# Performance work log

Hardware: AMD Instinct MI355X
Metric: run time of the kernel (lower is better)

The kernel has to match this reference:

```python
import jax, jax.numpy as jnp
import numpy as np
from jax import lax

NUM_MELS = 80
NQ = 256          # num_quants
WIN = 1024
HOP = 256
K_UP = 800        # upsample kernel
PAD_UP = K_UP + 4 * HOP - WIN   # = 800
RC = 120          # residual_channels
SC = 240          # skip_channels
KC = 2            # causal kernel
NB = 16           # num blocks
DILS = [1, 2, 4, 8, 16, 32, 64, 128] * 2
DN = ('NCH', 'OIH', 'NCH')


def conv1x1(x, w, b):
    # x: [B,C,T], w: [O,C], b: [O]
    return jnp.einsum('bct,oc->bot', x, w) + b[None, :, None]


def causal_conv(x, w, b, d):
    # x: [B,RC,T], w: [2RC,RC,KC], left-pad by d*(KC-1) -> causal, same length
    y = lax.conv_general_dilated(x, w, (1,), [(d * (KC - 1), 0)],
                                 rhs_dilation=(d,), dimension_numbers=DN)
    return y + b[None, :, None]


def setup_inputs() -> dict:
    key = jax.random.key(0)
    ks = jax.random.split(key, 20)
    s = 0.05
    n = jax.random.normal
    return {
        'waveforms': n(ks[0], (1, 40960), jnp.float32),
        'melspecs': n(ks[1], (1, NUM_MELS, 160), jnp.float32),
        # ConvTranspose-equivalent upsample weight, stored as direct conv weight [O,I,K]
        'up_w': s * n(ks[2], (NUM_MELS, NUM_MELS, K_UP), jnp.float32),
        'up_b': jnp.zeros((NUM_MELS,), jnp.float32),
        'in_w': s * n(ks[3], (RC, 1), jnp.float32),
        'in_b': jnp.zeros((RC,), jnp.float32),
        'blk_causal_w': s * n(ks[4], (NB, 2 * RC, RC, KC), jnp.float32),
        'blk_causal_b': jnp.zeros((NB, 2 * RC), jnp.float32),
        'blk_cond_w': s * n(ks[5], (NB, 2 * RC, NUM_MELS), jnp.float32),
        'blk_cond_b': jnp.zeros((NB, 2 * RC), jnp.float32),
        'blk_skip_w': s * n(ks[6], (NB, SC, RC), jnp.float32),
        'blk_skip_b': jnp.zeros((NB, SC), jnp.float32),
        'blk_res_w': s * n(ks[7], (NB, RC, RC), jnp.float32),
        'blk_res_b': jnp.zeros((NB, RC), jnp.float32),
        'h1_w': s * n(ks[8], (NQ, SC), jnp.float32),
        'h1_b': jnp.zeros((NQ,), jnp.float32),
        'h2_w': s * n(ks[9], (NQ, NQ), jnp.float32),
        'h2_b': jnp.zeros((NQ,), jnp.float32),
    }


def _forward(waveforms, melspecs, up_w, up_b, in_w, in_b,
             blk_causal_w, blk_causal_b, blk_cond_w, blk_cond_b,
             blk_skip_w, blk_skip_b, blk_res_w, blk_res_b,
             h1_w, h1_b, h2_w, h2_b):
    # ConvTranspose1d(stride=HOP, padding=PAD_UP) as lhs-dilated conv:
    # out_len = (F-1)*HOP + K_UP - 2*PAD_UP
    cond = lax.conv_general_dilated(
        melspecs, up_w, (1,), [(K_UP - 1 - PAD_UP, K_UP - 1 - PAD_UP)],
        lhs_dilation=(HOP,), dimension_numbers=DN) + up_b[None, :, None]
    L = min(waveforms.shape[-1], cond.shape[-1])
    wav = waveforms[..., :L]
    cond = cond[..., :L]

    res = conv1x1(wav[:, None, :], in_w, in_b)          # [B,RC,L]
    skip_sum = jnp.zeros((res.shape[0], SC, L), res.dtype)
    for i, d in enumerate(DILS):
        z = causal_conv(res, blk_causal_w[i], blk_causal_b[i], d) \
            + conv1x1(cond, blk_cond_w[i], blk_cond_b[i])  # [B,2RC,L]
        h = jnp.tanh(z[:, :RC]) * jax.nn.sigmoid(z[:, RC:])
        skip_sum = skip_sum + conv1x1(h, blk_skip_w[i], blk_skip_b[i])
        res = res + conv1x1(h, blk_res_w[i], blk_res_b[i])

    x = jax.nn.relu(skip_sum)
    x = jax.nn.relu(conv1x1(x, h1_w, h1_b))
    logits = conv1x1(x, h2_w, h2_b)                      # [B,NQ,L]
    return logits


def reference(waveforms, melspecs, up_w, up_b, in_w, in_b,
              blk_causal_w, blk_causal_b, blk_cond_w, blk_cond_b,
              blk_skip_w, blk_skip_b, blk_res_w, blk_res_b,
              h1_w, h1_b, h2_w, h2_b):
    return _forward(waveforms, melspecs, up_w, up_b, in_w, in_b,
                    blk_causal_w, blk_causal_b, blk_cond_w, blk_cond_b,
                    blk_skip_w, blk_skip_b, blk_res_w, blk_res_b,
                    h1_w, h1_b, h2_w, h2_b)
```

## Files before the change

kernel.cpp:

```cpp
#include <hip/hip_runtime.h>

#define L_LEN 39904
#define NT 624
#define RCH 120
#define SCH 240
#define CMEL 80
#define NQO 256
#define NBLK 16
#define KUP 800

typedef unsigned short u16;
typedef __attribute__((ext_vector_type(8))) short short8;
typedef __attribute__((ext_vector_type(4))) float f32x4;

#define MFMA(a, b, c) __builtin_amdgcn_mfma_f32_16x16x32_bf16((a), (b), (c), 0, 0, 0)

__device__ __forceinline__ u16 f2bf(float f) {
    unsigned u = __float_as_uint(f);
    u += 0x7FFFu + ((u >> 16) & 1u);
    return (u16)(u >> 16);
}
__device__ __forceinline__ unsigned pack2(float a, float b) {
    return (unsigned)f2bf(a) | ((unsigned)f2bf(b) << 16);
}
__device__ __forceinline__ float b16tof(u16 h) {
    return __uint_as_float((unsigned)h << 16);
}
__device__ __forceinline__ float gate(float a, float b) {
    float ea = __expf(2.f * a);
    float th = 1.f - 2.f * __builtin_amdgcn_rcpf(ea + 1.f);
    float sg = __builtin_amdgcn_rcpf(1.f + __expf(-b));
    return th * sg;
}

constexpr size_t O_CONDT = 0;
constexpr size_t O_RESA  = O_CONDT + 7023104;
constexpr size_t O_RESB  = O_RESA + 19153920;
constexpr size_t O_SKIP  = O_RESB + 19153920;
constexpr size_t O_ZFRAG = O_SKIP + 19153920;
constexpr size_t O_SKF   = O_ZFRAG + 2621440;
constexpr size_t O_RF    = O_SKF + 1048576;
constexpr size_t O_H1F   = O_RF + 524288;
constexpr size_t O_H2F   = O_H1F + 131072;
constexpr size_t O_UPF   = O_H2F + 131072;
constexpr size_t O_ZB    = O_UPF + 13107200;
constexpr size_t O_SKB   = O_ZB + 16384;

constexpr size_t H2_CONDT = 0;
constexpr size_t H2_RESF  = 7023104;
constexpr size_t H2_BFA   = H2_RESF + 19153920;
constexpr size_t H2_BFB   = H2_BFA + 9576960;
constexpr size_t H2_ZFRAG = H2_BFB + 9576960;
constexpr size_t H2_SKF   = H2_ZFRAG + 2621440;
constexpr size_t H2_RF    = H2_SKF + 1048576;
constexpr size_t H2_H1F   = H2_RF + 524288;
constexpr size_t H2_H2F   = H2_H1F + 131072;
constexpr size_t H2_ZB    = H2_H2F + 131072;
constexpr size_t H2_SKBS  = H2_ZB + 16384;
constexpr size_t H2_HALL  = H2_SKBS + 16384;
constexpr size_t H_BYTES  = (size_t)NBLK * L_LEN * 120 * 2;
constexpr size_t UPF_BYTES = 13107200;
constexpr size_t NEED_H = H2_HALL + (H_BYTES > UPF_BYTES ? H_BYTES : UPF_BYTES);

__global__ void k_prep_zfrag(const float* __restrict__ bc_w, const float* __restrict__ bq_w,
                             u16* __restrict__ dst) {
    int i = blockIdx.x * 256 + threadIdx.x;
    if (i >= NBLK * 10 * 16 * 512) return;
    int jj = i & 7, lane = (i >> 3) & 63, mt = (i >> 9) & 15;
    int rest = i >> 13, ks = rest % 10, blk = rest / 10;
    int m = mt * 16 + (lane & 15);
    int k = ks * 32 + ((lane >> 4) << 3) + jj;
    float v = 0.f;
    if (m < 240) {
        int o = (m & 1) ? (m >> 1) + 120 : (m >> 1);
        if (k < 120)       v = bc_w[((size_t)(blk * 240 + o) * 120 + k) * 2 + 0];
        else if (k < 240)  v = bc_w[((size_t)(blk * 240 + o) * 120 + (k - 120)) * 2 + 1];
        else               v = bq_w[(size_t)(blk * 240 + o) * 80 + (k - 240)];
    }
    dst[i] = f2bf(v);
}
__global__ void k_prep_skfrag(const float* __restrict__ bs_w, u16* __restrict__ dst) {
    int i = blockIdx.x * 256 + threadIdx.x;
    if (i >= NBLK * 4 * 16 * 512) return;
    int jj = i & 7, lane = (i >> 3) & 63, mt = (i >> 9) & 15;
    int rest = i >> 13, ks = rest & 3, blk = rest >> 2;
    int m = mt * 16 + (lane & 15);
    int k = ks * 32 + ((lane >> 4) << 3) + jj;
    float v = (m < 240 && k < 120) ? bs_w[(size_t)(blk * 240 + m) * 120 + k] : 0.f;
    dst[i] = f2bf(v);
}
__global__ void k_prep_rfrag(const float* __restrict__ br_w, u16* __restrict__ dst) {
    int i = blockIdx.x * 256 + threadIdx.x;
    if (i >= NBLK * 4 * 8 * 512) return;
    int jj = i & 7, lane = (i >> 3) & 63, mt = (i >> 9) & 7;
    int rest = i >> 12, ks = rest & 3, blk = rest >> 2;
    int m = mt * 16 + (lane & 15);
    int k = ks * 32 + ((lane >> 4) << 3) + jj;
    float v = (m < 120 && k < 120) ? br_w[(size_t)(blk * 120 + m) * 120 + k] : 0.f;
    dst[i] = f2bf(v);
}
__global__ void k_prep_h1frag(const float* __restrict__ h1_w, u16* __restrict__ dst) {
    int i = blockIdx.x * 256 + threadIdx.x;
    if (i >= 8 * 16 * 512) return;
    int jj = i & 7, lane = (i >> 3) & 63, mt = (i >> 9) & 15, ks = i >> 13;
    int m = mt * 16 + (lane & 15);
    int k = ks * 32 + ((lane >> 4) << 3) + jj;
    float v = (k < 240) ? h1_w[(size_t)m * 240 + k] : 0.f;
    dst[i] = f2bf(v);
}
__global__ void k_prep_h2frag(const float* __restrict__ h2_w, u16* __restrict__ dst) {
    int i = blockIdx.x * 256 + threadIdx.x;
    if (i >= 8 * 16 * 512) return;
    int jj = i & 7, lane = (i >> 3) & 63, mt = (i >> 9) & 15, ks = i >> 13;
    int m = mt * 16 + (lane & 15);
    int k = ks * 32 + ((lane >> 4) << 3) + jj;
    dst[i] = f2bf(h2_w[(size_t)m * 256 + k]);
}
__global__ void k_prep_upfrag(const float* __restrict__ up_w, u16* __restrict__ dst) {
    int i = blockIdx.x * 256 + threadIdx.x;
    if (i >= 256 * 10 * 5 * 512) return;
    int jj = i & 7, lane = (i >> 3) & 63;
    int rest = i >> 9;
    int mt = rest % 5; rest /= 5;
    int ks = rest % 10; int p = rest / 10;
    int m = mt * 16 + (lane & 15);
    int k = ks * 32 + ((lane >> 4) << 3) + jj;
    int c = k >> 2, j = k & 3;
    int r = (256 - ((p + 1) & 255)) & 255;
    int kk = r + 256 * j;
    float v = (m < 80 && kk < KUP) ? up_w[((size_t)m * 80 + c) * KUP + kk] : 0.f;
    dst[i] = f2bf(v);
}
__global__ void k_prep_zbias(const float* __restrict__ bc_b, const float* __restrict__ bq_b,
                             float* __restrict__ dst) {
    int i = blockIdx.x * 256 + threadIdx.x;
    if (i >= NBLK * 256) return;
    int m = i & 255, blk = i >> 8;
    float v = 0.f;
    if (m < 240) {
        int o = (m & 1) ? (m >> 1) + 120 : (m >> 1);
        v = bc_b[blk * 240 + o] + bq_b[blk * 240 + o];
    }
    dst[i] = v;
}
__global__ void k_prep_skbias(const float* __restrict__ bs_b, float* __restrict__ dst) {
    int i = blockIdx.x * 256 + threadIdx.x;
    if (i >= NBLK * 240) return;
    dst[i] = bs_b[i];
}
__global__ void k_prep_skbsum(const float* __restrict__ bs_b, float* __restrict__ dst) {
    int m = blockIdx.x * 256 + threadIdx.x;
    if (m >= 240) return;
    float s = 0.f;
    for (int i = 0; i < NBLK; i++) s += bs_b[i * 240 + m];
    dst[m] = s;
}
__global__ void k_res_initT(const float* __restrict__ wav, const float* __restrict__ in_w,
                            const float* __restrict__ in_b, float* __restrict__ resT) {
    int i = blockIdx.x * 256 + threadIdx.x;
    if (i >= L_LEN * RCH) return;
    int t = i / RCH, c = i % RCH;
    resT[i] = wav[t] * in_w[c] + in_b[c];
}
__global__ void k_res_initTb(const float* __restrict__ wav, const float* __restrict__ in_w,
                             const float* __restrict__ in_b, u16* __restrict__ resB) {
    int i = blockIdx.x * 256 + threadIdx.x;
    if (i >= L_LEN * RCH) return;
    int t = i / RCH, c = i % RCH;
    resB[i] = f2bf(wav[t] * in_w[c] + in_b[c]);
}

__global__ __launch_bounds__(256) void k_up(const float* __restrict__ mel,
        const u16* __restrict__ upf, const float* __restrict__ up_b,
        u16* __restrict__ condT) {
    __shared__ u16 s_ms[64 * 328];
    const int tid = threadIdx.x, l = tid & 63, w = tid >> 6;
    const int quad = l >> 4, tloc = l & 15;
    const int p = blockIdx.x, s0 = blockIdx.y * 64;
    for (int rr = 0; rr < 16; rr++) {
        int tt = w + 4 * rr;
        int sg = s0 + tt;
        #pragma unroll
        for (int base = 0; base < 320; base += 64) {
            int ck = base + l;
            int c = ck >> 2, j = ck & 3;
            int mi = 1 + j + sg;
            float v = (mi < 160) ? mel[c * 160 + mi] : 0.f;
            s_ms[tt * 328 + ck] = f2bf(v);
        }
    }
    __syncthreads();
    f32x4 acc[2][4];
    #pragma unroll
    for (int i = 0; i < 2; i++)
        #pragma unroll
        for (int n = 0; n < 4; n++) acc[i][n] = (f32x4){0.f, 0.f, 0.f, 0.f};
    const int nmt = (w == 0) ? 2 : 1;
    int mts[2]; mts[0] = w; mts[1] = 4;
    for (int ks = 0; ks < 10; ks++) {
        short8 b[4];
        int k0 = ks * 32 + quad * 8;
        #pragma unroll
        for (int n = 0; n < 4; n++)
            b[n] = *(const short8*)&s_ms[(n * 16 + tloc) * 328 + k0];
        const short8* ap = (const short8*)(upf) + ((size_t)p * 10 + ks) * 5 * 64;
        for (int i = 0; i < nmt; i++) {
            short8 a = ap[mts[i] * 64 + l];
            #pragma unroll
            for (int n = 0; n < 4; n++) acc[i][n] = MFMA(a, b[n], acc[i][n]);
        }
    }
    for (int i = 0; i < nmt; i++) {
        int o_base = mts[i] * 16 + quad * 4;
        float4 ub = *(const float4*)(up_b + o_base);
        float bb[4] = {ub.x, ub.y, ub.z, ub.w};
        #pragma unroll
        for (int n = 0; n < 4; n++) {
            int sg = s0 + n * 16 + tloc;
            int t = p + 256 * sg;
            if (t < L_LEN) {
                #pragma unroll
                for (int r = 0; r < 4; r++)
                    condT[(size_t)t * 88 + o_base + r] = f2bf(acc[i][n][r] + bb[r]);
            }
        }
    }
}

__global__ __launch_bounds__(512, 4) void k_block(
        const u16* __restrict__ condT, const float* __restrict__ resT_in,
        float* __restrict__ resT_out, u16* __restrict__ skipT,
        const u16* __restrict__ zfrag, const u16* __restrict__ skfrag,
        const u16* __restrict__ rfrag, const float* __restrict__ zbias,
        const float* __restrict__ skbias, const float* __restrict__ resb,
        int blk, int dil, int first) {
    __shared__ u16 s_x[64 * 328];
    u16* s_h = s_x;
    const int tid = threadIdx.x, l = tid & 63, w = tid >> 6;
    const int quad = l >> 4, tloc = l & 15;
    const int t0 = blockIdx.x * 64;
    const short8* zap = (const short8*)(zfrag) + (size_t)blk * 10 * 16 * 64;
    short8 a_cur[2], a_nxt[2];
    #pragma unroll
    for (int i = 0; i < 2; i++) a_cur[i] = zap[(size_t)(w * 2 + i) * 64 + l];
    for (int rr = 0; rr < 8; rr++) {
        int tt = w + 8 * rr;
        int tg = t0 + tt, tp = tg - dil;
        if (l < 60) {
            float2 pv = make_float2(0.f, 0.f), cv = make_float2(0.f, 0.f);
            if (tp >= 0 && tp < L_LEN) pv = *(const float2*)(resT_in + (size_t)tp * 120 + 2 * l);
            if (tg < L_LEN)            cv = *(const float2*)(resT_in + (size_t)tg * 120 + 2 * l);
            *(unsigned*)&s_x[tt * 328 + 2 * l]       = pack2(pv.x, pv.y);
            *(unsigned*)&s_x[tt * 328 + 120 + 2 * l] = pack2(cv.x, cv.y);
        }
        if (l < 40) {
            unsigned q = 0;
            if (tg < L_LEN) q = *(const unsigned*)(condT + (size_t)tg * 88 + 2 * l);
            *(unsigned*)&s_x[tt * 328 + 240 + 2 * l] = q;
        }
    }
    __syncthreads();
    f32x4 acc[2][4];
    #pragma unroll
    for (int i = 0; i < 2; i++)
        #pragma unroll
        for (int n = 0; n < 4; n++) acc[i][n] = (f32x4){0.f, 0.f, 0.f, 0.f};
    for (int ks = 0; ks < 10; ks++) {
        if (ks < 9) {
            #pragma unroll
            for (int i = 0; i < 2; i++)
                a_nxt[i] = zap[((size_t)(ks + 1) * 16 + w * 2 + i) * 64 + l];
        }
        int k0 = ks * 32 + quad * 8;
        short8 b[4];
        #pragma unroll
        for (int n = 0; n < 4; n++)
            b[n] = *(const short8*)&s_x[(n * 16 + tloc) * 328 + k0];
        #pragma unroll
        for (int i = 0; i < 2; i++)
            #pragma unroll
            for (int n = 0; n < 4; n++) acc[i][n] = MFMA(a_cur[i], b[n], acc[i][n]);
        #pragma unroll
        for (int i = 0; i < 2; i++) a_cur[i] = a_nxt[i];
    }
    const short8* sap = (const short8*)(skfrag) + (size_t)blk * 4 * 16 * 64;
    const short8* rap = (const short8*)(rfrag) + (size_t)blk * 4 * 8 * 64;
    short8 sa_c[2], sa_n[2], ra_c, ra_n;
    #pragma unroll
    for (int i = 0; i < 2; i++) sa_c[i] = sap[(size_t)(w * 2 + i) * 64 + l];
    ra_c = rap[(size_t)w * 64 + l];
    uint2 skp[2][4];
    if (!first) {
        #pragma unroll
        for (int i = 0; i < 2; i++) {
            int m_base = (w * 2 + i) * 16 + quad * 4;
            if (m_base < 240) {
                #pragma unroll
                for (int n = 0; n < 4; n++) {
                    int t = t0 + n * 16 + tloc;
                    if (t < L_LEN)
                        skp[i][n] = *(const uint2*)(skipT + (size_t)t * 240 + m_base);
                }
            }
        }
    }
    unsigned hu[2][4];
    #pragma unroll
    for (int i = 0; i < 2; i++) {
        int m_base = (w * 2 + i) * 16 + quad * 4;
        float4 bz4 = *(const float4*)(zbias + blk * 256 + m_base);
        #pragma unroll
        for (int n = 0; n < 4; n++) {
            float h0 = gate(acc[i][n][0] + bz4.x, acc[i][n][1] + bz4.y);
            float h1 = gate(acc[i][n][2] + bz4.z, acc[i][n][3] + bz4.w);
            hu[i][n] = pack2(h0, h1);
        }
    }
    __syncthreads();
    #pragma unroll
    for (int i = 0; i < 2; i++) {
        int j0 = (w * 2 + i) * 8 + quad * 2;
        #pragma unroll
        for (int n = 0; n < 4; n++)
            *(unsigned*)&s_h[(n * 16 + tloc) * 136 + j0] = hu[i][n];
    }
    __syncthreads();
    f32x4 sacc[2][4], racc[4];
    #pragma unroll
    for (int i = 0; i < 2; i++)
        #pragma unroll
        for (int n = 0; n < 4; n++) sacc[i][n] = (f32x4){0.f, 0.f, 0.f, 0.f};
    #pragma unroll
    for (int n = 0; n < 4; n++) racc[n] = (f32x4){0.f, 0.f, 0.f, 0.f};
    for (int ks = 0; ks < 4; ks++) {
        if (ks < 3) {
            #pragma unroll
            for (int i = 0; i < 2; i++)
                sa_n[i] = sap[((size_t)(ks + 1) * 16 + w * 2 + i) * 64 + l];
            ra_n = rap[((size_t)(ks + 1) * 8 + w) * 64 + l];
        }
        short8 b[4];
        int k0 = ks * 32 + quad * 8;
        #pragma unroll
        for (int n = 0; n < 4; n++)
            b[n] = *(const short8*)&s_h[(n * 16 + tloc) * 136 + k0];
        #pragma unroll
        for (int i = 0; i < 2; i++)
            #pragma unroll
            for (int n = 0; n < 4; n++) sacc[i][n] = MFMA(sa_c[i], b[n], sacc[i][n]);
        #pragma unroll
        for (int n = 0; n < 4; n++) racc[n] = MFMA(ra_c, b[n], racc[n]);
        #pragma unroll
        for (int i = 0; i < 2; i++) sa_c[i] = sa_n[i];
        ra_c = ra_n;
    }
    #pragma unroll
    for (int i = 0; i < 2; i++) {
        int m_base = (w * 2 + i) * 16 + quad * 4;
        if (m_base >= 240) continue;
        float4 sb4 = *(const float4*)(skbias + blk * 240 + m_base);
        #pragma unroll
        for (int n = 0; n < 4; n++) {
            int t = t0 + n * 16 + tloc;
            if (t >= L_LEN) continue;
            float x0 = sacc[i][n][0] + sb4.x;
            float x1 = sacc[i][n][1] + sb4.y;
            float x2 = sacc[i][n][2] + sb4.z;
            float x3 = sacc[i][n][3] + sb4.w;
            if (!first) {
                uint2 pv = skp[i][n];
                x0 += b16tof((u16)(pv.x & 0xFFFF));
                x1 += b16tof((u16)(pv.x >> 16));
                x2 += b16tof((u16)(pv.y & 0xFFFF));
                x3 += b16tof((u16)(pv.y >> 16));
            }
            uint2 ov;
            ov.x = pack2(x0, x1);
            ov.y = pack2(x2, x3);
            *(uint2*)(skipT + (size_t)t * 240 + m_base) = ov;
        }
    }
    {
        int m_base = w * 16 + quad * 4;
        if (m_base < 120) {
            float4 rb4 = *(const float4*)(resb + blk * 120 + m_base);
            #pragma unroll
            for (int n = 0; n < 4; n++) {
                int t = t0 + n * 16 + tloc;
                if (t >= L_LEN) continue;
                float4 cur = *(const float4*)(resT_in + (size_t)t * 120 + m_base);
                float4 o;
                o.x = cur.x + racc[n][0] + rb4.x;
                o.y = cur.y + racc[n][1] + rb4.y;
                o.z = cur.z + racc[n][2] + rb4.z;
                o.w = cur.w + racc[n][3] + rb4.w;
                *(float4*)(resT_out + (size_t)t * 120 + m_base) = o;
            }
        }
    }
}

__global__ __launch_bounds__(512, 4) void k_block_h4(
        const u16* __restrict__ condT,
        const u16* __restrict__ bfIn, u16* __restrict__ bfOut,
        u16* __restrict__ hout,
        const u16* __restrict__ zfrag, const u16* __restrict__ rfrag,
        const float* __restrict__ zbias, const float* __restrict__ resb,
        int blk, int dil) {
    __shared__ u16 s_x[64 * 328];
    u16* s_h = s_x;
    const int tid = threadIdx.x, l = tid & 63, w = tid >> 6;
    const int quad = l >> 4, tloc = l & 15;
    const int t0 = blockIdx.x * 64;
    const short8* zap = (const short8*)(zfrag) + (size_t)blk * 10 * 16 * 64;
    short8 a_cur[2], a_nxt[2];
    a_cur[0] = zap[(size_t)(w * 2 + 0) * 64 + l];
    a_cur[1] = zap[(size_t)(w * 2 + 1) * 64 + l];
    const uint2 Z2 = make_uint2(0u, 0u);
    for (int rr = 0; rr < 8; rr++) {
        int tt = w + 8 * rr, tg = t0 + tt;
        if (l < 30) {
            uint2 cv = (tg < L_LEN) ? *(const uint2*)(bfIn + (size_t)tg * 120 + 4 * l) : Z2;
            *(uint2*)&s_x[tt * 328 + 120 + 4 * l] = cv;
            if (tt < dil) {
                int tp = tg - dil;
                uint2 pv = (tp >= 0 && tp < L_LEN)
                    ? *(const uint2*)(bfIn + (size_t)tp * 120 + 4 * l) : Z2;
                *(uint2*)&s_x[tt * 328 + 4 * l] = pv;
            }
        } else if (l >= 32 && l < 54) {
            int c = l - 32;
            uint2 q = (tg < L_LEN) ? *(const uint2*)(condT + (size_t)tg * 88 + 4 * c) : Z2;
            *(uint2*)&s_x[tt * 328 + 240 + 4 * c] = q;
        }
    }
    __syncthreads();
    if (dil < 64) {
        for (int rr = 0; rr < 8; rr++) {
            int tt = w + 8 * rr;
            if (l < 30 && tt >= dil)
                *(uint2*)&s_x[tt * 328 + 4 * l] =
                    *(const uint2*)&s_x[(tt - dil) * 328 + 120 + 4 * l];
        }
        __syncthreads();
    }
    f32x4 acc[2][4];
    #pragma unroll
    for (int i = 0; i < 2; i++)
        #pragma unroll
        for (int n = 0; n < 4; n++) acc[i][n] = (f32x4){0.f, 0.f, 0.f, 0.f};
    for (int ks = 0; ks < 10; ks++) {
        if (ks < 9) {
            a_nxt[0] = zap[((size_t)(ks + 1) * 16 + w * 2 + 0) * 64 + l];
            a_nxt[1] = zap[((size_t)(ks + 1) * 16 + w * 2 + 1) * 64 + l];
        }
        int k0 = ks * 32 + quad * 8;
        short8 b[4];
        #pragma unroll
        for (int n = 0; n < 4; n++)
            b[n] = *(const short8*)&s_x[(n * 16 + tloc) * 328 + k0];
        #pragma unroll
        for (int i = 0; i < 2; i++)
            #pragma unroll
            for (int n = 0; n < 4; n++) acc[i][n] = MFMA(a_cur[i], b[n], acc[i][n]);
        a_cur[0] = a_nxt[0]; a_cur[1] = a_nxt[1];
    }
    const short8* rap = (const short8*)(rfrag) + (size_t)blk * 4 * 8 * 64;
    short8 ra_c = rap[(size_t)w * 64 + l], ra_n;
    const int m_r = w * 16 + quad * 4;
    uint2 curb[4];
    if (m_r < 120) {
        #pragma unroll
        for (int n = 0; n < 4; n++)
            curb[n] = *(const uint2*)&s_x[(n * 16 + tloc) * 328 + 120 + m_r];
    }
    unsigned hu[2][4];
    #pragma unroll
    for (int i = 0; i < 2; i++) {
        int m_base = (w * 2 + i) * 16 + quad * 4;
        float4 bz4 = *(const float4*)(zbias + blk * 256 + m_base);
        #pragma unroll
        for (int n = 0; n < 4; n++) {
            float h0 = gate(acc[i][n][0] + bz4.x, acc[i][n][1] + bz4.y);
            float h1 = gate(acc[i][n][2] + bz4.z, acc[i][n][3] + bz4.w);
            hu[i][n] = pack2(h0, h1);
        }
    }
    __syncthreads();
    #pragma unroll
    for (int i = 0; i < 2; i++) {
        int j0 = (w * 2 + i) * 8 + quad * 2;
        #pragma unroll
        for (int n = 0; n < 4; n++)
            *(unsigned*)&s_h[(n * 16 + tloc) * 136 + j0] = hu[i][n];
    }
    __syncthreads();
    for (int rr = 0; rr < 8; rr++) {
        int tt = w + 8 * rr, tg = t0 + tt;
        if (l < 60 && tg < L_LEN)
            *(unsigned*)&hout[(size_t)tg * 120 + 2 * l] =
                *(const unsigned*)&s_h[tt * 136 + 2 * l];
    }
    f32x4 racc[4];
    #pragma unroll
    for (int n = 0; n < 4; n++) racc[n] = (f32x4){0.f, 0.f, 0.f, 0.f};
    for (int ks = 0; ks < 4; ks++) {
        if (ks < 3) ra_n = rap[((size_t)(ks + 1) * 8 + w) * 64 + l];
        short8 b[4];
        int k0 = ks * 32 + quad * 8;
        #pragma unroll
        for (int n = 0; n < 4; n++)
            b[n] = *(const short8*)&s_h[(n * 16 + tloc) * 136 + k0];
        #pragma unroll
        for (int n = 0; n < 4; n++) racc[n] = MFMA(ra_c, b[n], racc[n]);
        ra_c = ra_n;
    }
    if (m_r < 120) {
        float4 rb4 = *(const float4*)(resb + blk * 120 + m_r);
        #pragma unroll
        for (int n = 0; n < 4; n++) {
            int t = t0 + n * 16 + tloc;
            if (t >= L_LEN) continue;
            float o0 = b16tof((u16)(curb[n].x & 0xFFFF)) + racc[n][0] + rb4.x;
            float o1 = b16tof((u16)(curb[n].x >> 16))    + racc[n][1] + rb4.y;
            float o2 = b16tof((u16)(curb[n].y & 0xFFFF)) + racc[n][2] + rb4.z;
            float o3 = b16tof((u16)(curb[n].y >> 16))    + racc[n][3] + rb4.w;
            uint2 hv;
            hv.x = pack2(o0, o1);
            hv.y = pack2(o2, o3);
            *(uint2*)(bfOut + (size_t)t * 120 + m_r) = hv;
        }
    }
}

__global__ __launch_bounds__(512, 4) void k_block_g4(
        const u16* __restrict__ condT,
        const u16* __restrict__ bfIn, u16* __restrict__ bfOut,
        u16* __restrict__ hall,
        const u16* __restrict__ zfrag, const u16* __restrict__ rfrag,
        const float* __restrict__ zbias, const float* __restrict__ resb,
        int base) {
    __shared__ u16 s_res[80 * 120];
    __shared__ u16 s_cond[80 * 88];
    __shared__ u16 s_h[80 * 136];
    const int tid = threadIdx.x, l = tid & 63, w = tid >> 6;
    const int quad = l >> 4, tloc = l & 15;
    const int t0 = blockIdx.x * 64;
    const uint2 Z2 = make_uint2(0u, 0u);
    for (int rr = 0; rr < 10; rr++) {
        int row = w + 8 * rr;
        int tg = t0 - 16 + row;
        bool ok = (tg >= 0 && tg < L_LEN);
        if (l < 30) {
            uint2 v = ok ? *(const uint2*)(bfIn + (size_t)tg * 120 + 4 * l) : Z2;
            *(uint2*)&s_res[row * 120 + 4 * l] = v;
        } else if (l >= 32 && l < 54) {
            int c = l - 32;
            uint2 q = ok ? *(const uint2*)(condT + (size_t)tg * 88 + 4 * c) : Z2;
            *(uint2*)&s_cond[row * 88 + 4 * c] = q;
        }
    }
    __syncthreads();
    const int m_r = w * 16 + quad * 4;
    for (int k = 0; k < 4; k++) {
        const int blk = base + k;
        const int d = 1 << k;
        const short8* zap = (const short8*)(zfrag) + (size_t)blk * 10 * 16 * 64;
        const short8* rap = (const short8*)(rfrag) + (size_t)blk * 4 * 8 * 64;
        u16* hout = hall + (size_t)blk * ((size_t)L_LEN * 120);
        short8 a_cur[2], a_nxt[2];
        a_cur[0] = zap[(size_t)(w * 2 + 0) * 64 + l];
        a_cur[1] = zap[(size_t)(w * 2 + 1) * 64 + l];
        f32x4 acc[2][5];
        #pragma unroll
        for (int i = 0; i < 2; i++)
            #pragma unroll
            for (int n = 0; n < 5; n++) acc[i][n] = (f32x4){0.f, 0.f, 0.f, 0.f};
        for (int ks = 0; ks < 10; ks++) {
            if (ks < 9) {
                a_nxt[0] = zap[((size_t)(ks + 1) * 16 + w * 2 + 0) * 64 + l];
                a_nxt[1] = zap[((size_t)(ks + 1) * 16 + w * 2 + 1) * 64 + l];
            }
            int k0 = ks * 32 + quad * 8;
            short8 b[5];
            #pragma unroll
            for (int n = 0; n < 5; n++) {
                int r = n * 16 + tloc;
                const u16* src;
                if (k0 < 120) {
                    int pr = r - d; if (pr < 0) pr = 0;
                    src = &s_res[pr * 120 + k0];
                } else if (k0 < 240) {
                    src = &s_res[r * 120 + (k0 - 120)];
                } else {
                    src = &s_cond[r * 88 + (k0 - 240)];
                }
                b[n] = *(const short8*)src;
            }
            #pragma unroll
            for (int i = 0; i < 2; i++)
                #pragma unroll
                for (int n = 0; n < 5; n++) acc[i][n] = MFMA(a_cur[i], b[n], acc[i][n]);
            a_cur[0] = a_nxt[0]; a_cur[1] = a_nxt[1];
        }
        unsigned hu[2][5];
        #pragma unroll
        for (int i = 0; i < 2; i++) {
            int m_base = (w * 2 + i) * 16 + quad * 4;
            float4 bz4 = *(const float4*)(zbias + blk * 256 + m_base);
            #pragma unroll
            for (int n = 0; n < 5; n++) {
                float h0 = gate(acc[i][n][0] + bz4.x, acc[i][n][1] + bz4.y);
                float h1 = gate(acc[i][n][2] + bz4.z, acc[i][n][3] + bz4.w);
                hu[i][n] = pack2(h0, h1);
            }
        }
        #pragma unroll
        for (int i = 0; i < 2; i++) {
            int j0 = (w * 2 + i) * 8 + quad * 2;
            #pragma unroll
            for (int n = 0; n < 5; n++)
                *(unsigned*)&s_h[(n * 16 + tloc) * 136 + j0] = hu[i][n];
        }
        __syncthreads();
        for (int rr = 0; rr < 8; rr++) {
            int row = 16 + w + 8 * rr;
            int tg = t0 + w + 8 * rr;
            if (l < 60 && tg < L_LEN)
                *(unsigned*)&hout[(size_t)tg * 120 + 2 * l] =
                    *(const unsigned*)&s_h[row * 136 + 2 * l];
        }
        f32x4 racc[5];
        #pragma unroll
        for (int n = 0; n < 5; n++) racc[n] = (f32x4){0.f, 0.f, 0.f, 0.f};
        short8 ra_c = rap[(size_t)w * 64 + l], ra_n;
        for (int ks = 0; ks < 4; ks++) {
            if (ks < 3) ra_n = rap[((size_t)(ks + 1) * 8 + w) * 64 + l];
            short8 b[5];
            int k0 = ks * 32 + quad * 8;
            #pragma unroll
            for (int n = 0; n < 5; n++)
                b[n] = *(const short8*)&s_h[(n * 16 + tloc) * 136 + k0];
            #pragma unroll
            for (int n = 0; n < 5; n++) racc[n] = MFMA(ra_c, b[n], racc[n]);
            ra_c = ra_n;
        }
        if (m_r < 120) {
            float4 rb4 = *(const float4*)(resb + blk * 120 + m_r);
            #pragma unroll
            for (int n = 0; n < 5; n++) {
                int row = n * 16 + tloc;
                int tg = t0 - 16 + row;
                if (tg < 0 || tg >= L_LEN) continue;
                uint2 cv = *(const uint2*)&s_res[row * 120 + m_r];
                float o0 = b16tof((u16)(cv.x & 0xFFFF)) + racc[n][0] + rb4.x;
                float o1 = b16tof((u16)(cv.x >> 16))    + racc[n][1] + rb4.y;
                float o2 = b16tof((u16)(cv.y & 0xFFFF)) + racc[n][2] + rb4.z;
                float o3 = b16tof((u16)(cv.y >> 16))    + racc[n][3] + rb4.w;
                uint2 hv;
                hv.x = pack2(o0, o1);
                hv.y = pack2(o2, o3);
                *(uint2*)&s_res[row * 120 + m_r] = hv;
            }
        }
        __syncthreads();
    }
    for (int rr = 0; rr < 8; rr++) {
        int row = 16 + w + 8 * rr;
        int tg = t0 + w + 8 * rr;
        if (l < 30 && tg < L_LEN)
            *(uint2*)(bfOut + (size_t)tg * 120 + 4 * l) =
                *(const uint2*)&s_res[row * 120 + 4 * l];
    }
}

__global__ __launch_bounds__(512, 4) void k_final(const u16* __restrict__ skipT,
        const u16* __restrict__ h1f, const u16* __restrict__ h2f,
        const float* __restrict__ h1_b, const float* __restrict__ h2_b,
        float* __restrict__ out) {
    __shared__ u16 s_m[64 * 264];
    const int tid = threadIdx.x, l = tid & 63, w = tid >> 6;
    const int quad = l >> 4, tloc = l & 15;
    const int t0 = blockIdx.x * 64;
    const short8* ap1 = (const short8*)h1f;
    short8 a_cur[2], a_nxt[2];
    #pragma unroll
    for (int i = 0; i < 2; i++) a_cur[i] = ap1[(size_t)(w * 2 + i) * 64 + l];
    for (int rr = 0; rr < 8; rr++) {
        int tt = w + 8 * rr;
        int tg = t0 + tt;
        uint2 v = make_uint2(0u, 0u);
        if (l < 60 && tg < L_LEN)
            v = *(const uint2*)(skipT + (size_t)tg * 240 + 4 * l);
        float x0 = fmaxf(b16tof((u16)(v.x & 0xFFFF)), 0.f);
        float x1 = fmaxf(b16tof((u16)(v.x >> 16)), 0.f);
        float x2 = fmaxf(b16tof((u16)(v.y & 0xFFFF)), 0.f);
        float x3 = fmaxf(b16tof((u16)(v.y >> 16)), 0.f);
        uint2 ov;
        ov.x = pack2(x0, x1);
        ov.y = pack2(x2, x3);
        *(uint2*)&s_m[tt * 264 + 4 * l] = ov;
    }
    __syncthreads();
    f32x4 acc[2][4];
    #pragma unroll
    for (int i = 0; i < 2; i++)
        #pragma unroll
        for (int n = 0; n < 4; n++) acc[i][n] = (f32x4){0.f, 0.f, 0.f, 0.f};
    for (int ks = 0; ks < 8; ks++) {
        if (ks < 7) {
            #pragma unroll
            for (int i = 0; i < 2; i++)
                a_nxt[i] = ap1[((size_t)(ks + 1) * 16 + w * 2 + i) * 64 + l];
        }
        short8 b[4];
        int k0 = ks * 32 + quad * 8;
        #pragma unroll
        for (int n = 0; n < 4; n++)
            b[n] = *(const short8*)&s_m[(n * 16 + tloc) * 264 + k0];
        #pragma unroll
        for (int i = 0; i < 2; i++)
            #pragma unroll
            for (int n = 0; n < 4; n++) acc[i][n] = MFMA(a_cur[i], b[n], acc[i][n]);
        #pragma unroll
        for (int i = 0; i < 2; i++) a_cur[i] = a_nxt[i];
    }
    unsigned ylo[2][4], yhi[2][4];
    #pragma unroll
    for (int i = 0; i < 2; i++) {
        int m_base = (w * 2 + i) * 16 + quad * 4;
        float4 b1 = *(const float4*)(h1_b + m_base);
        #pragma unroll
        for (int n = 0; n < 4; n++) {
            float y0 = fmaxf(acc[i][n][0] + b1.x, 0.f);
            float y1v = fmaxf(acc[i][n][1] + b1.y, 0.f);
            float y2 = fmaxf(acc[i][n][2] + b1.z, 0.f);
            float y3 = fmaxf(acc[i][n][3] + b1.w, 0.f);
            ylo[i][n] = pack2(y0, y1v);
            yhi[i][n] = pack2(y2, y3);
        }
    }
    const short8* ap2 = (const short8*)h2f;
    #pragma unroll
    for (int i = 0; i < 2; i++) a_cur[i] = ap2[(size_t)(w * 2 + i) * 64 + l];
    __syncthreads();
    #pragma unroll
    for (int i = 0; i < 2; i++) {
        int m_base = (w * 2 + i) * 16 + quad * 4;
        #pragma unroll
        for (int n = 0; n < 4; n++) {
            int t = n * 16 + tloc;
            *(unsigned*)&s_m[t * 264 + m_base]     = ylo[i][n];
            *(unsigned*)&s_m[t * 264 + m_base + 2] = yhi[i][n];
        }
    }
    __syncthreads();
    #pragma unroll
    for (int i = 0; i < 2; i++)
        #pragma unroll
        for (int n = 0; n < 4; n++) acc[i][n] = (f32x4){0.f, 0.f, 0.f, 0.f};
    for (int ks = 0; ks < 8; ks++) {
        if (ks < 7) {
            #pragma unroll
            for (int i = 0; i < 2; i++)
                a_nxt[i] = ap2[((size_t)(ks + 1) * 16 + w * 2 + i) * 64 + l];
        }
        short8 b[4];
        int k0 = ks * 32 + quad * 8;
        #pragma unroll
        for (int n = 0; n < 4; n++)
            b[n] = *(const short8*)&s_m[(n * 16 + tloc) * 264 + k0];
        #pragma unroll
        for (int i = 0; i < 2; i++)
            #pragma unroll
            for (int n = 0; n < 4; n++) acc[i][n] = MFMA(a_cur[i], b[n], acc[i][n]);
        #pragma unroll
        for (int i = 0; i < 2; i++) a_cur[i] = a_nxt[i];
    }
    #pragma unroll
    for (int i = 0; i < 2; i++) {
        int m_base = (w * 2 + i) * 16 + quad * 4;
        float4 b2 = *(const float4*)(h2_b + m_base);
        float bb[4] = {b2.x, b2.y, b2.z, b2.w};
        #pragma unroll
        for (int n = 0; n < 4; n++) {
            int t = t0 + n * 16 + tloc;
            if (t >= L_LEN) continue;
            #pragma unroll
            for (int r = 0; r < 4; r++)
                out[(size_t)(m_base + r) * L_LEN + t] = acc[i][n][r] + bb[r];
        }
    }
}

__global__ __launch_bounds__(512, 4) void k_final_h3(const u16* __restrict__ hall,
        const u16* __restrict__ skf, const u16* __restrict__ h1f,
        const u16* __restrict__ h2f, const float* __restrict__ skbsum,
        const float* __restrict__ h1_b, const float* __restrict__ h2_b,
        float* __restrict__ out) {
    __shared__ u16 smem[2 * 64 * 136];
    u16* s_m = smem;
    const int tid = threadIdx.x, l = tid & 63, w = tid >> 6;
    const int quad = l >> 4, tloc = l & 15;
    const int t0 = blockIdx.x * 64;
    const short8* sap = (const short8*)skf;

    unsigned ha[8], hb[8];
    auto LOADH = [&](unsigned (&reg)[8], int i) {
        const u16* hp = hall + (size_t)i * ((size_t)L_LEN * 120);
        #pragma unroll
        for (int rr = 0; rr < 8; rr++) {
            int tg = t0 + w + 8 * rr;
            reg[rr] = (l < 60 && tg < L_LEN)
                ? *(const unsigned*)&hp[(size_t)tg * 120 + 2 * l] : 0u;
        }
    };
    if (l >= 60) {
        #pragma unroll
        for (int rr = 0; rr < 8; rr++) {
            int row = w + 8 * rr;
            *(unsigned*)&smem[row * 136 + 2 * l] = 0u;
            *(unsigned*)&smem[64 * 136 + row * 136 + 2 * l] = 0u;
        }
    }
    LOADH(ha, 0);
    #pragma unroll
    for (int rr = 0; rr < 8; rr++)
        if (l < 60) *(unsigned*)&smem[(w + 8 * rr) * 136 + 2 * l] = ha[rr];
    LOADH(hb, 1);
    short8 sa_c[2], sa_n[2];
    sa_c[0] = sap[(size_t)(w * 2 + 0) * 64 + l];
    sa_c[1] = sap[(size_t)(w * 2 + 1) * 64 + l];
    f32x4 sacc[2][4];
    #pragma unroll
    for (int i = 0; i < 2; i++)
        #pragma unroll
        for (int n = 0; n < 4; n++) sacc[i][n] = (f32x4){0.f, 0.f, 0.f, 0.f};
    __syncthreads();
    #pragma unroll
    for (int i = 0; i < 16; i++) {
        u16* cur = smem + (i & 1) * (64 * 136);
        u16* nxt = smem + ((i + 1) & 1) * (64 * 136);
        unsigned (&wrg)[8] = (i & 1) ? ha : hb;
        unsigned (&lrg)[8] = (i & 1) ? hb : ha;
        if (i < 15) {
            #pragma unroll
            for (int rr = 0; rr < 8; rr++)
                if (l < 60) *(unsigned*)&nxt[(w + 8 * rr) * 136 + 2 * l] = wrg[rr];
        }
        if (i < 14) LOADH(lrg, i + 2);
        for (int ks = 0; ks < 4; ks++) {
            int g = i * 4 + ks;
            if (g < 63) {
                sa_n[0] = sap[((size_t)(g + 1) * 16 + w * 2 + 0) * 64 + l];
                sa_n[1] = sap[((size_t)(g + 1) * 16 + w * 2 + 1) * 64 + l];
            }
            int k0 = ks * 32 + quad * 8;
            short8 b[4];
            #pragma unroll
            for (int n = 0; n < 4; n++)
                b[n] = *(const short8*)&cur[(n * 16 + tloc) * 136 + k0];
            #pragma unroll
            for (int i2 = 0; i2 < 2; i2++)
                #pragma unroll
                for (int n = 0; n < 4; n++)
                    sacc[i2][n] = MFMA(sa_c[i2], b[n], sacc[i2][n]);
            sa_c[0] = sa_n[0]; sa_c[1] = sa_n[1];
        }
        __syncthreads();
    }
    const short8* ap1 = (const short8*)h1f;
    short8 a_cur[2], a_nxt[2];
    a_cur[0] = ap1[(size_t)(w * 2 + 0) * 64 + l];
    a_cur[1] = ap1[(size_t)(w * 2 + 1) * 64 + l];
    #pragma unroll
    for (int i2 = 0; i2 < 2; i2++) {
        int m_base = (w * 2 + i2) * 16 + quad * 4;
        float4 sb4 = make_float4(0.f, 0.f, 0.f, 0.f);
        bool valid = (m_base < 240);
        if (valid) sb4 = *(const float4*)(skbsum + m_base);
        #pragma unroll
        for (int n = 0; n < 4; n++) {
            float x0 = 0.f, x1 = 0.f, x2 = 0.f, x3 = 0.f;
            if (valid) {
                x0 = fmaxf(sacc[i2][n][0] + sb4.x, 0.f);
                x1 = fmaxf(sacc[i2][n][1] + sb4.y, 0.f);
                x2 = fmaxf(sacc[i2][n][2] + sb4.z, 0.f);
                x3 = fmaxf(sacc[i2][n][3] + sb4.w, 0.f);
            }
            int t = n * 16 + tloc;
            *(unsigned*)&s_m[t * 264 + m_base]     = pack2(x0, x1);
            *(unsigned*)&s_m[t * 264 + m_base + 2] = pack2(x2, x3);
        }
    }
    __syncthreads();
    f32x4 acc[2][4];
    #pragma unroll
    for (int i = 0; i < 2; i++)
        #pragma unroll
        for (int n = 0; n < 4; n++) acc[i][n] = (f32x4){0.f, 0.f, 0.f, 0.f};
    for (int ks = 0; ks < 8; ks++) {
        if (ks < 7) {
            #pragma unroll
            for (int i = 0; i < 2; i++)
                a_nxt[i] = ap1[((size_t)(ks + 1) * 16 + w * 2 + i) * 64 + l];
        }
        short8 b[4];
        int k0 = ks * 32 + quad * 8;
        #pragma unroll
        for (int n = 0; n < 4; n++)
            b[n] = *(const short8*)&s_m[(n * 16 + tloc) * 264 + k0];
        #pragma unroll
        for (int i = 0; i < 2; i++)
            #pragma unroll
            for (int n = 0; n < 4; n++) acc[i][n] = MFMA(a_cur[i], b[n], acc[i][n]);
        #pragma unroll
        for (int i = 0; i < 2; i++) a_cur[i] = a_nxt[i];
    }
    unsigned ylo[2][4], yhi[2][4];
    #pragma unroll
    for (int i = 0; i < 2; i++) {
        int m_base = (w * 2 + i) * 16 + quad * 4;
        float4 b1 = *(const float4*)(h1_b + m_base);
        #pragma unroll
        for (int n = 0; n < 4; n++) {
            float y0 = fmaxf(acc[i][n][0] + b1.x, 0.f);
            float y1v = fmaxf(acc[i][n][1] + b1.y, 0.f);
            float y2 = fmaxf(acc[i][n][2] + b1.z, 0.f);
            float y3 = fmaxf(acc[i][n][3] + b1.w, 0.f);
            ylo[i][n] = pack2(y0, y1v);
            yhi[i][n] = pack2(y2, y3);
        }
    }
    const short8* ap2 = (const short8*)h2f;
    #pragma unroll
    for (int i = 0; i < 2; i++) a_cur[i] = ap2[(size_t)(w * 2 + i) * 64 + l];
    __syncthreads();
    #pragma unroll
    for (int i = 0; i < 2; i++) {
        int m_base = (w * 2 + i) * 16 + quad * 4;
        #pragma unroll
        for (int n = 0; n < 4; n++) {
            int t = n * 16 + tloc;
            *(unsigned*)&s_m[t * 264 + m_base]     = ylo[i][n];
            *(unsigned*)&s_m[t * 264 + m_base + 2] = yhi[i][n];
        }
    }
    __syncthreads();
    #pragma unroll
    for (int i = 0; i < 2; i++)
        #pragma unroll
        for (int n = 0; n < 4; n++) acc[i][n] = (f32x4){0.f, 0.f, 0.f, 0.f};
    for (int ks = 0; ks < 8; ks++) {
        if (ks < 7) {
            #pragma unroll
            for (int i = 0; i < 2; i++)
                a_nxt[i] = ap2[((size_t)(ks + 1) * 16 + w * 2 + i) * 64 + l];
        }
        short8 b[4];
        int k0 = ks * 32 + quad * 8;
        #pragma unroll
        for (int n = 0; n < 4; n++)
            b[n] = *(const short8*)&s_m[(n * 16 + tloc) * 264 + k0];
        #pragma unroll
        for (int i = 0; i < 2; i++)
            #pragma unroll
            for (int n = 0; n < 4; n++) acc[i][n] = MFMA(a_cur[i], b[n], acc[i][n]);
        #pragma unroll
        for (int i = 0; i < 2; i++) a_cur[i] = a_nxt[i];
    }
    #pragma unroll
    for (int i = 0; i < 2; i++) {
        int m_base = (w * 2 + i) * 16 + quad * 4;
        float4 b2 = *(const float4*)(h2_b + m_base);
        float bb[4] = {b2.x, b2.y, b2.z, b2.w};
        #pragma unroll
        for (int n = 0; n < 4; n++) {
            int t = t0 + n * 16 + tloc;
            if (t >= L_LEN) continue;
            #pragma unroll
            for (int r = 0; r < 4; r++)
                out[(size_t)(m_base + r) * L_LEN + t] = acc[i][n][r] + bb[r];
        }
    }
}

extern "C" void kernel_launch(void* const* d_in, const int* in_sizes, int n_in,
                              void* d_out, int out_size, void* d_ws, size_t ws_size,
                              hipStream_t stream) {
    const float* wav   = (const float*)d_in[0];
    const float* mel   = (const float*)d_in[1];
    const float* up_w  = (const float*)d_in[2];
    const float* up_b  = (const float*)d_in[3];
    const float* in_w  = (const float*)d_in[4];
    const float* in_b  = (const float*)d_in[5];
    const float* bc_w  = (const float*)d_in[6];
    const float* bc_b  = (const float*)d_in[7];
    const float* bq_w  = (const float*)d_in[8];
    const float* bq_b  = (const float*)d_in[9];
    const float* bs_w  = (const float*)d_in[10];
    const float* bs_b  = (const float*)d_in[11];
    const float* br_w  = (const float*)d_in[12];
    const float* br_b  = (const float*)d_in[13];
    const float* h1_w  = (const float*)d_in[14];
    const float* h1_b  = (const float*)d_in[15];
    const float* h2_w  = (const float*)d_in[16];
    const float* h2_b  = (const float*)d_in[17];

    char* wsb = (char*)d_ws;
    const bool use_h = (ws_size >= NEED_H);

    if (use_h) {
        u16*   condT = (u16*)(wsb + H2_CONDT);
        u16*   bfA   = (u16*)(wsb + H2_BFA);
        u16*   bfB   = (u16*)(wsb + H2_BFB);
        u16*   zfrag = (u16*)(wsb + H2_ZFRAG);
        u16*   skf   = (u16*)(wsb + H2_SKF);
        u16*   rf    = (u16*)(wsb + H2_RF);
        u16*   h1f   = (u16*)(wsb + H2_H1F);
        u16*   h2f   = (u16*)(wsb + H2_H2F);
        float* zb    = (float*)(wsb + H2_ZB);
        float* skbs  = (float*)(wsb + H2_SKBS);
        u16*   hall  = (u16*)(wsb + H2_HALL);
        u16*   upf   = (u16*)(wsb + H2_HALL);

        k_prep_zfrag <<<5120, 256, 0, stream>>>(bc_w, bq_w, zfrag);
        k_prep_skfrag<<<2048, 256, 0, stream>>>(bs_w, skf);
        k_prep_rfrag <<<1024, 256, 0, stream>>>(br_w, rf);
        k_prep_h1frag<<<256, 256, 0, stream>>>(h1_w, h1f);
        k_prep_h2frag<<<256, 256, 0, stream>>>(h2_w, h2f);
        k_prep_upfrag<<<25600, 256, 0, stream>>>(up_w, upf);
        k_prep_zbias <<<16, 256, 0, stream>>>(bc_b, bq_b, zb);
        k_prep_skbsum<<<1, 256, 0, stream>>>(bs_b, skbs);
        k_res_initTb <<<(L_LEN * RCH + 255) / 256, 256, 0, stream>>>(wav, in_w, in_b, bfA);
        k_up<<<dim3(256, 3), 256, 0, stream>>>(mel, upf, up_b, condT);

        u16* rin = bfA;
        u16* rout = bfB;
        k_block_g4<<<NT, 512, 0, stream>>>(condT, rin, rout, hall, zfrag, rf, zb, br_b, 0);
        { u16* t = rin; rin = rout; rout = t; }
        for (int i = 4; i < 8; i++) {
            k_block_h4<<<NT, 512, 0, stream>>>(condT, rin, rout,
                                               hall + (size_t)i * (size_t)L_LEN * 120,
                                               zfrag, rf, zb, br_b, i, 1 << (i & 7));
            u16* t = rin; rin = rout; rout = t;
        }
        k_block_g4<<<NT, 512, 0, stream>>>(condT, rin, rout, hall, zfrag, rf, zb, br_b, 8);
        { u16* t = rin; rin = rout; rout = t; }
        for (int i = 12; i < 16; i++) {
            k_block_h4<<<NT, 512, 0, stream>>>(condT, rin, rout,
                                               hall + (size_t)i * (size_t)L_LEN * 120,
                                               zfrag, rf, zb, br_b, i, 1 << (i & 7));
            u16* t = rin; rin = rout; rout = t;
        }
        k_final_h3<<<NT, 512, 0, stream>>>(hall, skf, h1f, h2f, skbs, h1_b, h2_b,
                                           (float*)d_out);
    } else {
        u16*   condT = (u16*)(wsb + O_CONDT);
        float* resA  = (float*)(wsb + O_RESA);
        float* resB  = (float*)(wsb + O_RESB);
        u16*   skipT = (u16*)(wsb + O_SKIP);
        u16*   zfrag = (u16*)(wsb + O_ZFRAG);
        u16*   skf   = (u16*)(wsb + O_SKF);
        u16*   rf    = (u16*)(wsb + O_RF);
        u16*   h1f   = (u16*)(wsb + O_H1F);
        u16*   h2f   = (u16*)(wsb + O_H2F);
        u16*   upf   = (u16*)(wsb + O_UPF);
        float* zb    = (float*)(wsb + O_ZB);
        float* skb   = (float*)(wsb + O_SKB);

        k_prep_zfrag <<<5120, 256, 0, stream>>>(bc_w, bq_w, zfrag);
        k_prep_skfrag<<<2048, 256, 0, stream>>>(bs_w, skf);
        k_prep_rfrag <<<1024, 256, 0, stream>>>(br_w, rf);
        k_prep_h1frag<<<256, 256, 0, stream>>>(h1_w, h1f);
        k_prep_h2frag<<<256, 256, 0, stream>>>(h2_w, h2f);
        k_prep_upfrag<<<25600, 256, 0, stream>>>(up_w, upf);
        k_prep_zbias <<<16, 256, 0, stream>>>(bc_b, bq_b, zb);
        k_prep_skbias<<<15, 256, 0, stream>>>(bs_b, skb);
        k_res_initT  <<<(L_LEN * RCH + 255) / 256, 256, 0, stream>>>(wav, in_w, in_b, resA);
        k_up<<<dim3(256, 3), 256, 0, stream>>>(mel, upf, up_b, condT);

        for (int i = 0; i < NBLK; i++) {
            int d = 1 << (i & 7);
            const float* rin = (i & 1) ? resB : resA;
            float* rout      = (i & 1) ? resA : resB;
            k_block<<<NT, 512, 0, stream>>>(condT, rin, rout, skipT, zfrag, skf, rf,
                                            zb, skb, br_b, i, d, (i == 0) ? 1 : 0);
        }
        k_final<<<NT, 512, 0, stream>>>(skipT, h1f, h2f, h1_b, h2_b, (float*)d_out);
    }
}
```

Measured before the change: 704.9 us.

## Fuse skip projection into grouped block kernel, emit partial skip sums

The grouped 4-layer kernel now computes the skip 1x1 projection in registers from the gated activations it already holds in shared memory. It writes one bf16 partial skip sum per group instead of storing every layer's h to global memory. The final kernel then loads only the 8 remaining layers' h plus two partial-sum buffers, which cuts global traffic and skip MFMA work in the final pass. The cost is extra MFMAs and registers in the block kernel, plus an additional bf16 rounding of the partial skip sums.

```diff
diff --git a/kernel.cpp b/kernel.cpp
--- a/kernel.cpp
+++ b/kernel.cpp
@@ -536,8 +536,9 @@
 __global__ __launch_bounds__(512, 4) void k_block_g4(
         const u16* __restrict__ condT,
         const u16* __restrict__ bfIn, u16* __restrict__ bfOut,
-        u16* __restrict__ hall,
-        const u16* __restrict__ zfrag, const u16* __restrict__ rfrag,
+        u16* __restrict__ skpart,
+        const u16* __restrict__ zfrag, const u16* __restrict__ skfrag,
+        const u16* __restrict__ rfrag,
         const float* __restrict__ zbias, const float* __restrict__ resb,
         int base) {
     __shared__ u16 s_res[80 * 120];
@@ -562,12 +563,17 @@
     }
     __syncthreads();
     const int m_r = w * 16 + quad * 4;
+    f32x4 skacc[2][4];
+    #pragma unroll
+    for (int i = 0; i < 2; i++)
+        #pragma unroll
+        for (int n = 0; n < 4; n++) skacc[i][n] = (f32x4){0.f, 0.f, 0.f, 0.f};
     for (int k = 0; k < 4; k++) {
         const int blk = base + k;
         const int d = 1 << k;
         const short8* zap = (const short8*)(zfrag) + (size_t)blk * 10 * 16 * 64;
         const short8* rap = (const short8*)(rfrag) + (size_t)blk * 4 * 8 * 64;
-        u16* hout = hall + (size_t)blk * ((size_t)L_LEN * 120);
+        const short8* sap = (const short8*)(skfrag) + (size_t)blk * 4 * 16 * 64;
         short8 a_cur[2], a_nxt[2];
         a_cur[0] = zap[(size_t)(w * 2 + 0) * 64 + l];
         a_cur[1] = zap[(size_t)(w * 2 + 1) * 64 + l];
@@ -623,19 +629,19 @@
                 *(unsigned*)&s_h[(n * 16 + tloc) * 136 + j0] = hu[i][n];
         }
         __syncthreads();
-        for (int rr = 0; rr < 8; rr++) {
-            int row = 16 + w + 8 * rr;
-            int tg = t0 + w + 8 * rr;
-            if (l < 60 && tg < L_LEN)
-                *(unsigned*)&hout[(size_t)tg * 120 + 2 * l] =
-                    *(const unsigned*)&s_h[row * 136 + 2 * l];
-        }
         f32x4 racc[5];
         #pragma unroll
         for (int n = 0; n < 5; n++) racc[n] = (f32x4){0.f, 0.f, 0.f, 0.f};
         short8 ra_c = rap[(size_t)w * 64 + l], ra_n;
+        short8 sa_c[2], sa_n[2];
+        sa_c[0] = sap[(size_t)(w * 2 + 0) * 64 + l];
+        sa_c[1] = sap[(size_t)(w * 2 + 1) * 64 + l];
         for (int ks = 0; ks < 4; ks++) {
-            if (ks < 3) ra_n = rap[((size_t)(ks + 1) * 8 + w) * 64 + l];
+            if (ks < 3) {
+                ra_n = rap[((size_t)(ks + 1) * 8 + w) * 64 + l];
+                sa_n[0] = sap[((size_t)(ks + 1) * 16 + w * 2 + 0) * 64 + l];
+                sa_n[1] = sap[((size_t)(ks + 1) * 16 + w * 2 + 1) * 64 + l];
+            }
             short8 b[5];
             int k0 = ks * 32 + quad * 8;
             #pragma unroll
@@ -643,7 +649,13 @@
                 b[n] = *(const short8*)&s_h[(n * 16 + tloc) * 136 + k0];
             #pragma unroll
             for (int n = 0; n < 5; n++) racc[n] = MFMA(ra_c, b[n], racc[n]);
+            #pragma unroll
+            for (int i = 0; i < 2; i++)
+                #pragma unroll
+                for (int n = 0; n < 4; n++)
+                    skacc[i][n] = MFMA(sa_c[i], b[n + 1], skacc[i][n]);
             ra_c = ra_n;
+            sa_c[0] = sa_n[0]; sa_c[1] = sa_n[1];
         }
         if (m_r < 120) {
             float4 rb4 = *(const float4*)(resb + blk * 120 + m_r);
@@ -664,6 +676,20 @@
             }
         }
         __syncthreads();
+    }
+    #pragma unroll
+    for (int i = 0; i < 2; i++) {
+        int m_base = (w * 2 + i) * 16 + quad * 4;
+        if (m_base >= 240) continue;
+        #pragma unroll
+        for (int n = 0; n < 4; n++) {
+            int t = t0 + n * 16 + tloc;
+            if (t >= L_LEN) continue;
+            uint2 ov;
+            ov.x = pack2(skacc[i][n][0], skacc[i][n][1]);
+            ov.y = pack2(skacc[i][n][2], skacc[i][n][3]);
+            *(uint2*)(skpart + (size_t)t * 240 + m_base) = ov;
+        }
     }
     for (int rr = 0; rr < 8; rr++) {
         int row = 16 + w + 8 * rr;
@@ -793,7 +819,8 @@
     }
 }
 
-__global__ __launch_bounds__(512, 4) void k_final_h3(const u16* __restrict__ hall,
+__global__ __launch_bounds__(512, 4) void k_final_h5(const u16* __restrict__ hall,
+        const u16* __restrict__ p0, const u16* __restrict__ p1,
         const u16* __restrict__ skf, const u16* __restrict__ h1f,
         const u16* __restrict__ h2f, const float* __restrict__ skbsum,
         const float* __restrict__ h1_b, const float* __restrict__ h2_b,
@@ -804,10 +831,11 @@
     const int quad = l >> 4, tloc = l & 15;
     const int t0 = blockIdx.x * 64;
     const short8* sap = (const short8*)skf;
+    const int LL[8] = {4, 5, 6, 7, 12, 13, 14, 15};
 
     unsigned ha[8], hb[8];
-    auto LOADH = [&](unsigned (&reg)[8], int i) {
-        const u16* hp = hall + (size_t)i * ((size_t)L_LEN * 120);
+    auto LOADH = [&](unsigned (&reg)[8], int layer) {
+        const u16* hp = hall + (size_t)layer * ((size_t)L_LEN * 120);
         #pragma unroll
         for (int rr = 0; rr < 8; rr++) {
             int tg = t0 + w + 8 * rr;
@@ -823,14 +851,14 @@
             *(unsigned*)&smem[64 * 136 + row * 136 + 2 * l] = 0u;
         }
     }
-    LOADH(ha, 0);
+    LOADH(ha, LL[0]);
     #pragma unroll
     for (int rr = 0; rr < 8; rr++)
         if (l < 60) *(unsigned*)&smem[(w + 8 * rr) * 136 + 2 * l] = ha[rr];
-    LOADH(hb, 1);
+    LOADH(hb, LL[1]);
     short8 sa_c[2], sa_n[2];
-    sa_c[0] = sap[(size_t)(w * 2 + 0) * 64 + l];
-    sa_c[1] = sap[(size_t)(w * 2 + 1) * 64 + l];
+    sa_c[0] = sap[((size_t)(LL[0] * 4) * 16 + w * 2 + 0) * 64 + l];
+    sa_c[1] = sap[((size_t)(LL[0] * 4) * 16 + w * 2 + 1) * 64 + l];
     f32x4 sacc[2][4];
     #pragma unroll
     for (int i = 0; i < 2; i++)
@@ -838,22 +866,23 @@
         for (int n = 0; n < 4; n++) sacc[i][n] = (f32x4){0.f, 0.f, 0.f, 0.f};
     __syncthreads();
     #pragma unroll
-    for (int i = 0; i < 16; i++) {
+    for (int i = 0; i < 8; i++) {
         u16* cur = smem + (i & 1) * (64 * 136);
         u16* nxt = smem + ((i + 1) & 1) * (64 * 136);
         unsigned (&wrg)[8] = (i & 1) ? ha : hb;
         unsigned (&lrg)[8] = (i & 1) ? hb : ha;
-        if (i < 15) {
+        if (i < 7) {
             #pragma unroll
             for (int rr = 0; rr < 8; rr++)
                 if (l < 60) *(unsigned*)&nxt[(w + 8 * rr) * 136 + 2 * l] = wrg[rr];
         }
-        if (i < 14) LOADH(lrg, i + 2);
+        if (i < 6) LOADH(lrg, LL[i + 2]);
         for (int ks = 0; ks < 4; ks++) {
-            int g = i * 4 + ks;
-            if (g < 63) {
-                sa_n[0] = sap[((size_t)(g + 1) * 16 + w * 2 + 0) * 64 + l];
-                sa_n[1] = sap[((size_t)(g + 1) * 16 + w * 2 + 1) * 64 + l];
+            int idx = i * 4 + ks + 1;
+            if (idx < 32) {
+                int gn = LL[idx >> 2] * 4 + (idx & 3);
+                sa_n[0] = sap[((size_t)gn * 16 + w * 2 + 0) * 64 + l];
+                sa_n[1] = sap[((size_t)gn * 16 + w * 2 + 1) * 64 + l];
             }
             int k0 = ks * 32 + quad * 8;
             short8 b[4];
@@ -882,15 +911,26 @@
         #pragma unroll
         for (int n = 0; n < 4; n++) {
             float x0 = 0.f, x1 = 0.f, x2 = 0.f, x3 = 0.f;
+            int t = t0 + n * 16 + tloc;
             if (valid) {
-                x0 = fmaxf(sacc[i2][n][0] + sb4.x, 0.f);
-                x1 = fmaxf(sacc[i2][n][1] + sb4.y, 0.f);
-                x2 = fmaxf(sacc[i2][n][2] + sb4.z, 0.f);
-                x3 = fmaxf(sacc[i2][n][3] + sb4.w, 0.f);
+                float s0 = sacc[i2][n][0], s1 = sacc[i2][n][1];
+                float s2 = sacc[i2][n][2], s3 = sacc[i2][n][3];
+                if (t < L_LEN) {
+                    uint2 pv0 = *(const uint2*)(p0 + (size_t)t * 240 + m_base);
+                    uint2 pv1 = *(const uint2*)(p1 + (size_t)t * 240 + m_base);
+                    s0 += b16tof((u16)(pv0.x & 0xFFFF)) + b16tof((u16)(pv1.x & 0xFFFF));
+                    s1 += b16tof((u16)(pv0.x >> 16))    + b16tof((u16)(pv1.x >> 16));
+                    s2 += b16tof((u16)(pv0.y & 0xFFFF)) + b16tof((u16)(pv1.y & 0xFFFF));
+                    s3 += b16tof((u16)(pv0.y >> 16))    + b16tof((u16)(pv1.y >> 16));
+                }
+                x0 = fmaxf(s0 + sb4.x, 0.f);
+                x1 = fmaxf(s1 + sb4.y, 0.f);
+                x2 = fmaxf(s2 + sb4.z, 0.f);
+                x3 = fmaxf(s3 + sb4.w, 0.f);
             }
-            int t = n * 16 + tloc;
-            *(unsigned*)&s_m[t * 264 + m_base]     = pack2(x0, x1);
-            *(unsigned*)&s_m[t * 264 + m_base + 2] = pack2(x2, x3);
+            int tt = n * 16 + tloc;
+            *(unsigned*)&s_m[tt * 264 + m_base]     = pack2(x0, x1);
+            *(unsigned*)&s_m[tt * 264 + m_base + 2] = pack2(x2, x3);
         }
     }
     __syncthreads();
@@ -1023,6 +1063,8 @@
         float* skbs  = (float*)(wsb + H2_SKBS);
         u16*   hall  = (u16*)(wsb + H2_HALL);
         u16*   upf   = (u16*)(wsb + H2_HALL);
+        u16*   P0    = hall;
+        u16*   P1    = hall + (size_t)2 * L_LEN * 120;
 
         k_prep_zfrag <<<5120, 256, 0, stream>>>(bc_w, bq_w, zfrag);
         k_prep_skfrag<<<2048, 256, 0, stream>>>(bs_w, skf);
@@ -1037,7 +1079,7 @@
 
         u16* rin = bfA;
         u16* rout = bfB;
-        k_block_g4<<<NT, 512, 0, stream>>>(condT, rin, rout, hall, zfrag, rf, zb, br_b, 0);
+        k_block_g4<<<NT, 512, 0, stream>>>(condT, rin, rout, P0, zfrag, skf, rf, zb, br_b, 0);
         { u16* t = rin; rin = rout; rout = t; }
         for (int i = 4; i < 8; i++) {
             k_block_h4<<<NT, 512, 0, stream>>>(condT, rin, rout,
@@ -1045,7 +1087,7 @@
                                                zfrag, rf, zb, br_b, i, 1 << (i & 7));
             u16* t = rin; rin = rout; rout = t;
         }
-        k_block_g4<<<NT, 512, 0, stream>>>(condT, rin, rout, hall, zfrag, rf, zb, br_b, 8);
+        k_block_g4<<<NT, 512, 0, stream>>>(condT, rin, rout, P1, zfrag, skf, rf, zb, br_b, 8);
         { u16* t = rin; rin = rout; rout = t; }
         for (int i = 12; i < 16; i++) {
             k_block_h4<<<NT, 512, 0, stream>>>(condT, rin, rout,
@@ -1053,8 +1095,8 @@
                                                zfrag, rf, zb, br_b, i, 1 << (i & 7));
             u16* t = rin; rin = rout; rout = t;
         }
-        k_final_h3<<<NT, 512, 0, stream>>>(hall, skf, h1f, h2f, skbs, h1_b, h2_b,
-                                           (float*)d_out);
+        k_final_h5<<<NT, 512, 0, stream>>>(hall, P0, P1, skf, h1f, h2f, skbs,
+                                           h1_b, h2_b, (float*)d_out);
     } else {
         u16*   condT = (u16*)(wsb + O_CONDT);
         float* resA  = (float*)(wsb + O_RESA);
```

New measurement: 714.8 us. No clear change (+1.4%).
